# Optimization experiments

Hardware: AMD Instinct MI355X
Metric: run time of the kernel (lower is better)

The kernel has to match this reference:

```python
import jax, jax.numpy as jnp
import numpy as np

CHANNEL = 1
ALPHA = 1.0
EPS = 1e-10
SHAPE = (1, CHANNEL, 160, 192, 160)


def _sobel_kernels(channel):
    s2 = np.array([[-1., 0., 1.], [-2., 0., 2.], [-1., 0., 1.]], dtype=np.float32)
    # sobel.repeat(channel,1,3,1,1): 2D kernel tiled along depth -> k[d,h,w] = s2[h,w]
    kx = np.tile(s2[None, :, :], (3, 1, 1))
    ky = np.tile(s2.T[None, :, :], (3, 1, 1))
    kz = np.array([[[-1., -1., -1.], [-2., -2., -2.], [-1., -1., -1.]],
                   [[0., 0., 0.], [0., 0., 0.], [0., 0., 0.]],
                   [[1., 1., 1.], [2., 2., 2.], [1., 1., 1.]]], dtype=np.float32)
    def rep(k):  # -> [channel, 1, 3, 3, 3] for depthwise conv
        return jnp.asarray(np.tile(k[None, None], (channel, 1, 1, 1, 1)))
    return rep(kx), rep(ky), rep(kz)


def _conv3d(x, k, channel):
    # torch F.conv3d (cross-correlation), padding=1, groups=channel
    return jax.lax.conv_general_dilated(
        x, k, window_strides=(1, 1, 1), padding=((1, 1), (1, 1), (1, 1)),
        dimension_numbers=('NCDHW', 'OIDHW', 'NCDHW'),
        feature_group_count=channel)


def setup_inputs() -> dict:
    key = jax.random.key(0)
    k1, k2, k3 = jax.random.split(key, 3)
    M = jax.random.normal(k1, SHAPE, dtype=jnp.float32)
    S = jax.random.normal(k2, SHAPE, dtype=jnp.float32)
    flow = jax.random.normal(k3, (SHAPE[0], 3) + SHAPE[2:], dtype=jnp.float32)
    return {"M": M, "S": S, "flow": flow}


def reference(M, S, flow):
    kx, ky, kz = _sobel_kernels(CHANNEL)
    Idiff = M - S
    Sx = _conv3d(S, kx, CHANNEL)
    Sy = _conv3d(S, ky, CHANNEL)
    Sz = _conv3d(S, kz, CHANNEL)
    Mx = _conv3d(M, kx, CHANNEL)
    My = _conv3d(M, ky, CHANNEL)
    Mz = _conv3d(M, kz, CHANNEL)
    Sxyz_mag = Sx ** 2 + Sy ** 2 + Sz ** 2
    Mxyz_mag = Mx ** 2 + My ** 2 + Mz ** 2
    denom_S = Sxyz_mag + (ALPHA ** 2) * Idiff ** 2 + 1e-10
    denom_M = Mxyz_mag + (ALPHA ** 2) * Idiff ** 2 + 1e-10
    Ux = Idiff * (Sx / denom_S + Mx / denom_M)
    Uy = Idiff * (Sy / denom_S + My / denom_M)
    Uz = Idiff * (Sz / denom_S + Mz / denom_M)
    demons_ori_xz = jnp.arctan(Ux / (Uz + EPS))
    demons_ori_yz = jnp.arctan(Uy / (Uz + EPS))
    flow_ori_xz = jnp.arctan(flow[:, 0] / (flow[:, 2] + EPS))
    flow_ori_yz = jnp.arctan(flow[:, 1] / (flow[:, 2] + EPS))
    ori_error = jnp.mean((flow_ori_xz - demons_ori_xz) ** 2) + \
                jnp.mean((flow_ori_yz - demons_ori_yz) ** 2)
    return ori_error
```

## Files before the change

### kernel.cpp

```cpp
#include <hip/hip_runtime.h>
#include <math.h>

#define DD 160
#define HH 192
#define WW 160
#define TW 16
#define TH 4
#define BW 32
#define BH 8
#define TD 8
#define HW (HH * WW)
#define NVOX (DD * HW)
#define HTW 18
#define HTH 6
#define LSTR 24
#define HALO (HTH * HTW)
#define WBUF (HTH * LSTR)

__device__ __forceinline__ float atan_fast(float r) {
    float ar = fabsf(r);
    float inv = __builtin_amdgcn_rcpf(ar);
    bool big = ar > 1.0f;
    float x = big ? inv : ar;
    float x2 = x * x;
    float p = fmaf(x2, fmaf(x2, fmaf(x2, fmaf(x2, fmaf(x2,
              -0.0117212f, 0.05265332f), -0.11643287f), 0.19354346f),
              -0.33262347f), 0.99997726f);
    p *= x;
    float res = big ? (1.57079632679489662f - p) : p;
    return copysignf(res, r);
}

__global__ __launch_bounds__(256) void demons_ori_kernel(
    const float* __restrict__ Mv, const float* __restrict__ Sv,
    const float* __restrict__ flow, float* __restrict__ out)
{
    __shared__ float buf[4][2][2][WBUF];
    __shared__ float redbuf[4];

    const int tid = threadIdx.x;
    const int wid = tid >> 6;
    const int lane = tid & 63;
    const int tw = lane & 15;
    const int th = lane >> 4;
    const int w0 = blockIdx.x * BW + (wid & 1) * TW;
    const int h0 = blockIdx.y * BH + (wid >> 1) * TH;
    const int d0 = blockIdx.z * TD;

    const bool has1 = (lane < HALO - 64);
    int idx0, gb0, idx1 = 0, gb1 = 0;
    bool ok0, ok1 = false;
    {
        int i = lane;
        int hh = i / HTW, ww = i - HTW * hh;
        int gh = h0 + hh - 1, gw = w0 + ww - 1;
        idx0 = hh * LSTR + ww;
        ok0 = (gh >= 0 && gh < HH && gw >= 0 && gw < WW);
        gb0 = gh * WW + gw;
        if (has1) {
            i = lane + 64;
            hh = i / HTW; ww = i - HTW * hh;
            gh = h0 + hh - 1; gw = w0 + ww - 1;
            idx1 = hh * LSTR + ww;
            ok1 = (gh >= 0 && gh < HH && gw >= 0 && gw < WW);
            gb1 = gh * WW + gw;
        }
    }

    float pS0 = 0.f, pM0 = 0.f, pS1 = 0.f, pM1 = 0.f;

    auto issue = [&](int d) {
        const bool din = (d >= 0) && (d < DD);
        const size_t base = (size_t)d * HW;
        pS0 = (din && ok0) ? Sv[base + gb0] : 0.f;
        pM0 = (din && ok0) ? Mv[base + gb0] : 0.f;
        pS1 = (din && ok1) ? Sv[base + gb1] : 0.f;
        pM1 = (din && ok1) ? Mv[base + gb1] : 0.f;
    };
    auto commit = [&](int d) {
        float* __restrict__ bS = &buf[wid][d & 1][0][0];
        float* __restrict__ bM = &buf[wid][d & 1][1][0];
        bS[idx0] = pS0; bM[idx0] = pM0;
        if (has1) { bS[idx1] = pS1; bM[idx1] = pM1; }
    };

    const int rb = th * LSTR + tw;
    auto partials = [&](int par, float pq[2][4]) {
        #pragma unroll
        for (int f = 0; f < 2; ++f) {
            const float* __restrict__ b = &buf[wid][par][f][0];
            const float* r0 = b + rb;
            const float* r1 = r0 + LSTR;
            const float* r2 = r1 + LSTR;
            float v00 = r0[0], v01 = r0[1], v02 = r0[2];
            float v10 = r1[0], v11 = r1[1], v12 = r1[2];
            float v20 = r2[0], v21 = r2[1], v22 = r2[2];
            pq[f][0] = (v02 + 2.f * v12 + v22) - (v00 + 2.f * v10 + v20);
            pq[f][1] = (v20 + 2.f * v21 + v22) - (v00 + 2.f * v01 + v02);
            pq[f][2] = (v00 + v01 + v02) + 2.f * (v10 + v11 + v12)
                     + (v20 + v21 + v22);
            pq[f][3] = v11;
        }
    };

    float Pm[2][4], P0[2][4], Pp[2][4];

    issue(d0 - 1);
    commit(d0 - 1);
    issue(d0);
    partials((d0 - 1) & 1, Pm);
    commit(d0);
    issue(d0 + 1);
    partials(d0 & 1, P0);

    const size_t voff0 = (size_t)(h0 + th) * WW + (w0 + tw);
    float fFx = flow[(size_t)d0 * HW + voff0];
    float fFy = flow[(size_t)NVOX + (size_t)d0 * HW + voff0];
    float fFz = flow[2 * (size_t)NVOX + (size_t)d0 * HW + voff0];

    float lsum = 0.f;

    #pragma unroll
    for (int dd = 0; dd < TD; ++dd) {
        const int d = d0 + dd;
        commit(d + 1);
        float nFx = 0.f, nFy = 0.f, nFz = 0.f;
        if (dd < TD - 1) {
            issue(d + 2);
            size_t foff = (size_t)(d + 1) * HW + voff0;
            nFx = flow[foff];
            nFy = flow[(size_t)NVOX + foff];
            nFz = flow[2 * (size_t)NVOX + foff];
        }
        partials((d + 1) & 1, Pp);

        float idf = P0[1][3] - P0[0][3];
        float i2 = idf * idf + 1e-10f;
        float gxS = Pm[0][0] + P0[0][0] + Pp[0][0];
        float gyS = Pm[0][1] + P0[0][1] + Pp[0][1];
        float gzS = Pp[0][2] - Pm[0][2];
        float gxM = Pm[1][0] + P0[1][0] + Pp[1][0];
        float gyM = Pm[1][1] + P0[1][1] + Pp[1][1];
        float gzM = Pp[1][2] - Pm[1][2];
        float denS = gxS * gxS + gyS * gyS + gzS * gzS + i2;
        float denM = gxM * gxM + gyM * gyM + gzM * gzM + i2;
        float rS = __builtin_amdgcn_rcpf(denS);
        float rM = __builtin_amdgcn_rcpf(denM);
        float Ux = idf * (gxS * rS + gxM * rM);
        float Uy = idf * (gyS * rS + gyM * rM);
        float Uz = idf * (gzS * rS + gzM * rM);
        float rz = __builtin_amdgcn_rcpf(Uz + 1e-10f);
        float dxz = atan_fast(Ux * rz);
        float dyz = atan_fast(Uy * rz);

        float rf = __builtin_amdgcn_rcpf(fFz + 1e-10f);
        float fxz = atan_fast(fFx * rf);
        float fyz = atan_fast(fFy * rf);

        float e1 = fxz - dxz;
        float e2 = fyz - dyz;
        lsum += e1 * e1 + e2 * e2;

        #pragma unroll
        for (int f = 0; f < 2; ++f)
            #pragma unroll
            for (int q = 0; q < 4; ++q) {
                Pm[f][q] = P0[f][q];
                P0[f][q] = Pp[f][q];
            }
        fFx = nFx; fFy = nFy; fFz = nFz;
    }

    #pragma unroll
    for (int o = 32; o > 0; o >>= 1)
        lsum += __shfl_down(lsum, o, 64);
    if (lane == 0)
        redbuf[wid] = lsum;
    __syncthreads();
    if (tid == 0) {
        float s = redbuf[0] + redbuf[1] + redbuf[2] + redbuf[3];
        atomicAdd(out, s * (1.0f / (float)NVOX));
    }
}

extern "C" void kernel_launch(void* const* d_in, const int* in_sizes, int n_in,
                              void* d_out, int out_size, void* d_ws, size_t ws_size,
                              hipStream_t stream) {
    const float* Mv   = (const float*)d_in[0];
    const float* Sv   = (const float*)d_in[1];
    const float* flow = (const float*)d_in[2];
    float* out = (float*)d_out;

    hipMemsetAsync(out, 0, sizeof(float), stream);

    dim3 grid(WW / BW, HH / BH, DD / TD);
    demons_ori_kernel<<<grid, dim3(256), 0, stream>>>(Mv, Sv, flow, out);
}
```

Measured before the change: 152.3 us.

## Reshape per-wave tiles to 32x2 with contiguous halo staging and occupancy hint

Result: slower. 161.7 us (+6.1%).

```diff
diff --git a/kernel.cpp b/kernel.cpp
--- a/kernel.cpp
+++ b/kernel.cpp
@@ -4,16 +4,15 @@
 #define DD 160
 #define HH 192
 #define WW 160
-#define TW 16
-#define TH 4
-#define BW 32
+#define TW 32
+#define TH 2
 #define BH 8
 #define TD 8
 #define HW (HH * WW)
 #define NVOX (DD * HW)
-#define HTW 18
-#define HTH 6
-#define LSTR 24
+#define HTW 34
+#define HTH 4
+#define LSTR 34
 #define HALO (HTH * HTW)
 #define WBUF (HTH * LSTR)
 
@@ -31,7 +30,7 @@
     return copysignf(res, r);
 }
 
-__global__ __launch_bounds__(256) void demons_ori_kernel(
+__global__ __launch_bounds__(256, 6) void demons_ori_kernel(
     const float* __restrict__ Mv, const float* __restrict__ Sv,
     const float* __restrict__ flow, float* __restrict__ out)
 {
@@ -41,33 +40,36 @@
     const int tid = threadIdx.x;
     const int wid = tid >> 6;
     const int lane = tid & 63;
-    const int tw = lane & 15;
-    const int th = lane >> 4;
-    const int w0 = blockIdx.x * BW + (wid & 1) * TW;
-    const int h0 = blockIdx.y * BH + (wid >> 1) * TH;
+    const int tw = lane & 31;
+    const int th = lane >> 5;
+    const int w0 = blockIdx.x * TW;
+    const int h0 = blockIdx.y * BH + wid * TH;
     const int d0 = blockIdx.z * TD;
 
-    const bool has1 = (lane < HALO - 64);
-    int idx0, gb0, idx1 = 0, gb1 = 0;
-    bool ok0, ok1 = false;
+    const bool has2 = (lane < HALO - 128);
+    int gb0, gb1, gb2 = 0;
+    bool ok0, ok1, ok2 = false;
     {
         int i = lane;
         int hh = i / HTW, ww = i - HTW * hh;
         int gh = h0 + hh - 1, gw = w0 + ww - 1;
-        idx0 = hh * LSTR + ww;
         ok0 = (gh >= 0 && gh < HH && gw >= 0 && gw < WW);
         gb0 = gh * WW + gw;
-        if (has1) {
-            i = lane + 64;
+        i = lane + 64;
+        hh = i / HTW; ww = i - HTW * hh;
+        gh = h0 + hh - 1; gw = w0 + ww - 1;
+        ok1 = (gh >= 0 && gh < HH && gw >= 0 && gw < WW);
+        gb1 = gh * WW + gw;
+        if (has2) {
+            i = lane + 128;
             hh = i / HTW; ww = i - HTW * hh;
             gh = h0 + hh - 1; gw = w0 + ww - 1;
-            idx1 = hh * LSTR + ww;
-            ok1 = (gh >= 0 && gh < HH && gw >= 0 && gw < WW);
-            gb1 = gh * WW + gw;
+            ok2 = (gh >= 0 && gh < HH && gw >= 0 && gw < WW);
+            gb2 = gh * WW + gw;
         }
     }
 
-    float pS0 = 0.f, pM0 = 0.f, pS1 = 0.f, pM1 = 0.f;
+    float pS0 = 0.f, pM0 = 0.f, pS1 = 0.f, pM1 = 0.f, pS2 = 0.f, pM2 = 0.f;
 
     auto issue = [&](int d) {
         const bool din = (d >= 0) && (d < DD);
@@ -76,12 +78,15 @@
         pM0 = (din && ok0) ? Mv[base + gb0] : 0.f;
         pS1 = (din && ok1) ? Sv[base + gb1] : 0.f;
         pM1 = (din && ok1) ? Mv[base + gb1] : 0.f;
+        pS2 = (din && ok2) ? Sv[base + gb2] : 0.f;
+        pM2 = (din && ok2) ? Mv[base + gb2] : 0.f;
     };
     auto commit = [&](int d) {
         float* __restrict__ bS = &buf[wid][d & 1][0][0];
         float* __restrict__ bM = &buf[wid][d & 1][1][0];
-        bS[idx0] = pS0; bM[idx0] = pM0;
-        if (has1) { bS[idx1] = pS1; bM[idx1] = pM1; }
+        bS[lane] = pS0;       bM[lane] = pM0;
+        bS[lane + 64] = pS1;  bM[lane + 64] = pM1;
+        if (has2) { bS[lane + 128] = pS2; bM[lane + 128] = pM2; }
     };
 
     const int rb = th * LSTR + tw;
@@ -120,7 +125,7 @@
 
     float lsum = 0.f;
 
-    #pragma unroll
+    #pragma unroll 2
     for (int dd = 0; dd < TD; ++dd) {
         const int d = d0 + dd;
         commit(d + 1);
@@ -193,6 +198,6 @@
 
     hipMemsetAsync(out, 0, sizeof(float), stream);
 
-    dim3 grid(WW / BW, HH / BH, DD / TD);
+    dim3 grid(WW / TW, HH / BH, DD / TD);
     demons_ori_kernel<<<grid, dim3(256), 0, stream>>>(Mv, Sv, flow, out);
 }
```
